# Kernel optimization log

Measured on AMD Instinct MI355X. Metric: run time of the kernel, lower is better.

Reference implementation:

```python
import jax, jax.numpy as jnp
import numpy as np

N_NODES = 100000
N_EDGES = 1600000
H_FEATS = 64


def setup_inputs() -> dict:
    key = jax.random.key(0)
    k_h, k_src, k_dst, k_w1, k_b1, k_w2, k_b2 = jax.random.split(key, 7)
    h = jax.random.normal(k_h, (N_NODES, H_FEATS), dtype=jnp.float32)
    src = jax.random.randint(k_src, (N_EDGES,), 0, N_NODES, dtype=jnp.int64)
    dst = jax.random.randint(k_dst, (N_EDGES,), 0, N_NODES, dtype=jnp.int64)
    # Linear params (torch Linear: y = x @ W.T + b). Store as [in, out] for jnp.
    lim1 = 1.0 / np.sqrt(2 * H_FEATS)
    W1 = jax.random.uniform(k_w1, (2 * H_FEATS, H_FEATS), minval=-lim1, maxval=lim1, dtype=jnp.float32)
    b1 = jax.random.uniform(k_b1, (H_FEATS,), minval=-lim1, maxval=lim1, dtype=jnp.float32)
    lim2 = 1.0 / np.sqrt(H_FEATS)
    W2 = jax.random.uniform(k_w2, (H_FEATS, 1), minval=-lim2, maxval=lim2, dtype=jnp.float32)
    b2 = jax.random.uniform(k_b2, (1,), minval=-lim2, maxval=lim2, dtype=jnp.float32)
    return {"h": h, "src": src, "dst": dst, "W1": W1, "b1": b1, "W2": W2, "b2": b2}


def reference(h, src, dst, W1, b1, W2, b2):
    # Gather src/dst node features per edge, avoid materializing the concat by
    # splitting W1 into the src-half and dst-half of the contraction.
    W1s, W1d = W1[:H_FEATS], W1[H_FEATS:]            # each [h, h]
    h_src = h[src]                                    # [E, h]
    h_dst = h[dst]                                    # [E, h]
    hidden = jax.nn.relu(h_src @ W1s + h_dst @ W1d + b1)  # [E, h]
    score = (hidden @ W2 + b2)[:, 0]                  # [E]
    return score
```

## Files before the change

kernel.cpp:

```cpp
#include <hip/hip_runtime.h>
#include <hip/hip_fp16.h>


#define HF   64
#define PADH 136
#define TPB  2

typedef __attribute__((ext_vector_type(8))) short bf16x8;
typedef __attribute__((ext_vector_type(4))) float f32x4;

__device__ __forceinline__ short f2bf(float x) {
    unsigned u = __builtin_bit_cast(unsigned, x);
    unsigned r = (u + 0x7fffu + ((u >> 16) & 1u)) >> 16;
    return (short)r;
}

__global__ __launch_bounds__(256) void node_proj_kernel(
    const float* __restrict__ h, const float* __restrict__ W1,
    const float* __restrict__ b1, __half* __restrict__ P,
    __half* __restrict__ Q, int n_nodes)
{
    __shared__ __half eb[64 * PADH];

    const int tid  = threadIdx.x;
    const int wave = tid >> 6;
    const int lane = tid & 63;
    const int q    = lane >> 4;
    const int n    = lane & 15;

    bf16x8 bfrag[8][2];
    #pragma unroll
    for (int t = 0; t < 8; ++t) {
        const float* wb = W1 + ((t >= 4) ? HF * HF : 0) + (t & 3) * 16 + n;
        #pragma unroll
        for (int kb = 0; kb < 2; ++kb) {
            #pragma unroll
            for (int j = 0; j < 8; ++j)
                bfrag[t][kb][j] = f2bf(wb[(kb * 32 + q * 8 + j) * HF]);
        }
    }
    const float bias_n = b1[0 * 16 + n];
    const float bias_n1 = b1[1 * 16 + n];
    const float bias_n2 = b1[2 * 16 + n];
    const float bias_n3 = b1[3 * 16 + n];

    for (int it = 0; it < TPB; ++it) {
        const int tile = blockIdx.x * TPB + it;
        const int n0   = tile * 64;
        if (n0 >= n_nodes) break;
        const int nrow = (n_nodes - n0 < 64) ? (n_nodes - n0) : 64;

        bf16x8 a0, a1;
        {
            int row = n0 + wave * 16 + n;
            if (row >= n_nodes) row = n_nodes - 1;
            const float* hr = h + (size_t)row * HF + q * 8;
            const float4 u0 = *(const float4*)(hr);
            const float4 u1 = *(const float4*)(hr + 4);
            const float4 v0 = *(const float4*)(hr + 32);
            const float4 v1 = *(const float4*)(hr + 36);
            a0[0] = f2bf(u0.x); a0[1] = f2bf(u0.y); a0[2] = f2bf(u0.z); a0[3] = f2bf(u0.w);
            a0[4] = f2bf(u1.x); a0[5] = f2bf(u1.y); a0[6] = f2bf(u1.z); a0[7] = f2bf(u1.w);
            a1[0] = f2bf(v0.x); a1[1] = f2bf(v0.y); a1[2] = f2bf(v0.z); a1[3] = f2bf(v0.w);
            a1[4] = f2bf(v1.x); a1[5] = f2bf(v1.y); a1[6] = f2bf(v1.z); a1[7] = f2bf(v1.w);
        }

        f32x4 acc[8];
        #pragma unroll
        for (int t = 0; t < 8; ++t) {
            acc[t] = (f32x4){0.f, 0.f, 0.f, 0.f};
            acc[t] = __builtin_amdgcn_mfma_f32_16x16x32_bf16(a0, bfrag[t][0], acc[t], 0, 0, 0);
            acc[t] = __builtin_amdgcn_mfma_f32_16x16x32_bf16(a1, bfrag[t][1], acc[t], 0, 0, 0);
        }

        if (it > 0) __syncthreads();

        #pragma unroll
        for (int t = 0; t < 8; ++t) {
            const float bb = (t == 0) ? bias_n : (t == 1) ? bias_n1
                           : (t == 2) ? bias_n2 : (t == 3) ? bias_n3 : 0.0f;
            #pragma unroll
            for (int r = 0; r < 4; ++r) {
                const int row = wave * 16 + q * 4 + r;
                eb[row * PADH + t * 16 + n] = __float2half(acc[t][r] + bb);
            }
        }
        __syncthreads();

        #pragma unroll
        for (int s = 0; s < 4; ++s) {
            const int idx  = tid + s * 256;
            const int row  = idx >> 4;
            const int part = idx & 15;
            if (row < nrow) {
                const uint4 v = *(const uint4*)&eb[row * PADH + part * 8];
                __half* dstp = (part < 8)
                    ? (P + (size_t)(n0 + row) * HF + part * 8)
                    : (Q + (size_t)(n0 + row) * HF + (part - 8) * 8);
                *(uint4*)dstp = v;
            }
        }
    }
}

__device__ __forceinline__ float dot8_relu(uint4 pv, uint4 qv, float4 wa, float4 wb) {
    const __half2* ph = (const __half2*)&pv;
    const __half2* qh = (const __half2*)&qv;
    const float2 p0 = __half22float2(ph[0]), q0 = __half22float2(qh[0]);
    const float2 p1 = __half22float2(ph[1]), q1 = __half22float2(qh[1]);
    const float2 p2 = __half22float2(ph[2]), q2 = __half22float2(qh[2]);
    const float2 p3 = __half22float2(ph[3]), q3 = __half22float2(qh[3]);
    float acc = 0.f;
    acc = fmaf(fmaxf(p0.x + q0.x, 0.f), wa.x, acc);
    acc = fmaf(fmaxf(p0.y + q0.y, 0.f), wa.y, acc);
    acc = fmaf(fmaxf(p1.x + q1.x, 0.f), wa.z, acc);
    acc = fmaf(fmaxf(p1.y + q1.y, 0.f), wa.w, acc);
    acc = fmaf(fmaxf(p2.x + q2.x, 0.f), wb.x, acc);
    acc = fmaf(fmaxf(p2.y + q2.y, 0.f), wb.y, acc);
    acc = fmaf(fmaxf(p3.x + q3.x, 0.f), wb.z, acc);
    acc = fmaf(fmaxf(p3.y + q3.y, 0.f), wb.w, acc);
    return acc;
}

__device__ __forceinline__ float red8(float v) {
    v += __shfl_xor(v, 4, 8);
    v += __shfl_xor(v, 2, 8);
    v += __shfl_xor(v, 1, 8);
    return v;
}

__global__ __launch_bounds__(256) void edge_score_kernel(
    const __half* __restrict__ P, const __half* __restrict__ Q,
    const int* __restrict__ src, const int* __restrict__ dst,
    const float* __restrict__ W2, const float* __restrict__ b2,
    float* __restrict__ out, int n_edges)
{
    const int tid   = blockIdx.x * 256 + threadIdx.x;
    const int sub   = threadIdx.x & 7;
    const int group = tid >> 3;
    const int j0    = sub * 8;
    const int e0    = group * 8;
    if (e0 >= n_edges) return;

    const float4 w2a = *(const float4*)(W2 + j0);
    const float4 w2b = *(const float4*)(W2 + j0 + 4);
    const float bias2 = b2[0];

    if (e0 + 8 <= n_edges) {
        const int4 sA = *(const int4*)(src + e0);
        const int4 sB = *(const int4*)(src + e0 + 4);
        const int4 dA = *(const int4*)(dst + e0);
        const int4 dB = *(const int4*)(dst + e0 + 4);

        const uint4 p0 = *(const uint4*)(P + (size_t)sA.x * HF + j0);
        const uint4 p1 = *(const uint4*)(P + (size_t)sA.y * HF + j0);
        const uint4 p2 = *(const uint4*)(P + (size_t)sA.z * HF + j0);
        const uint4 p3 = *(const uint4*)(P + (size_t)sA.w * HF + j0);
        const uint4 p4 = *(const uint4*)(P + (size_t)sB.x * HF + j0);
        const uint4 p5 = *(const uint4*)(P + (size_t)sB.y * HF + j0);
        const uint4 p6 = *(const uint4*)(P + (size_t)sB.z * HF + j0);
        const uint4 p7 = *(const uint4*)(P + (size_t)sB.w * HF + j0);
        const uint4 q0 = *(const uint4*)(Q + (size_t)dA.x * HF + j0);
        const uint4 q1 = *(const uint4*)(Q + (size_t)dA.y * HF + j0);
        const uint4 q2 = *(const uint4*)(Q + (size_t)dA.z * HF + j0);
        const uint4 q3 = *(const uint4*)(Q + (size_t)dA.w * HF + j0);
        const uint4 q4 = *(const uint4*)(Q + (size_t)dB.x * HF + j0);
        const uint4 q5 = *(const uint4*)(Q + (size_t)dB.y * HF + j0);
        const uint4 q6 = *(const uint4*)(Q + (size_t)dB.z * HF + j0);
        const uint4 q7 = *(const uint4*)(Q + (size_t)dB.w * HF + j0);

        float s0 = red8(dot8_relu(p0, q0, w2a, w2b));
        float s1 = red8(dot8_relu(p1, q1, w2a, w2b));
        float s2 = red8(dot8_relu(p2, q2, w2a, w2b));
        float s3 = red8(dot8_relu(p3, q3, w2a, w2b));
        float s4 = red8(dot8_relu(p4, q4, w2a, w2b));
        float s5 = red8(dot8_relu(p5, q5, w2a, w2b));
        float s6 = red8(dot8_relu(p6, q6, w2a, w2b));
        float s7 = red8(dot8_relu(p7, q7, w2a, w2b));

        if (sub == 0) {
            *(float4*)(out + e0)     = make_float4(s0 + bias2, s1 + bias2,
                                                   s2 + bias2, s3 + bias2);
            *(float4*)(out + e0 + 4) = make_float4(s4 + bias2, s5 + bias2,
                                                   s6 + bias2, s7 + bias2);
        }
    } else {
        for (int e = e0; e < n_edges; ++e) {
            const int s = src[e];
            const int d = dst[e];
            const uint4 pv = *(const uint4*)(P + (size_t)s * HF + j0);
            const uint4 qv = *(const uint4*)(Q + (size_t)d * HF + j0);
            float sc = red8(dot8_relu(pv, qv, w2a, w2b));
            if (sub == 0) out[e] = sc + bias2;
        }
    }
}

extern "C" void kernel_launch(void* const* d_in, const int* in_sizes, int n_in,
                              void* d_out, int out_size, void* d_ws, size_t ws_size,
                              hipStream_t stream) {
    const float* h   = (const float*)d_in[0];
    const int*   src = (const int*)d_in[1];
    const int*   dst = (const int*)d_in[2];
    const float* W1  = (const float*)d_in[3];
    const float* b1  = (const float*)d_in[4];
    const float* W2  = (const float*)d_in[5];
    const float* b2  = (const float*)d_in[6];
    float* out = (float*)d_out;

    const int n_nodes = in_sizes[0] / HF;
    const int n_edges = in_sizes[1];

    __half* P = (__half*)d_ws;
    __half* Q = P + (size_t)n_nodes * HF;

    const int ntiles   = (n_nodes + 63) / 64;
    const int nblocks1 = (ntiles + TPB - 1) / TPB;
    node_proj_kernel<<<nblocks1, 256, 0, stream>>>(h, W1, b1, P, Q, n_nodes);

    const int ngroups  = (n_edges + 7) / 8;
    const int nblocks2 = (ngroups + 31) / 32;
    edge_score_kernel<<<nblocks2, 256, 0, stream>>>(P, Q, src, dst, W2, b2, out, n_edges);
}
```

Before: 146.7 us.

## Quantize per-node projections to int8 with per-row scales for edge gathers

The node projection kernel now stores P and Q as 8-bit offset-quantized values with a per-node float scale, instead of fp16. The edge kernel gathers half as many bytes per edge and dequantizes inline before the ReLU and W2 dot product. The aim is to cut the random-gather memory traffic that dominates the edge kernel. The cost is extra scale loads and shuffles, more ALU work per element, and quantization error that may exceed tolerance.

Measured after the change: 147.8 us. No clear change (+0.8%).

```diff
diff --git a/kernel.cpp b/kernel.cpp
--- a/kernel.cpp
+++ b/kernel.cpp
@@ -2,9 +2,9 @@
 #include <hip/hip_fp16.h>
 
 
-#define HF   64
-#define PADH 136
-#define TPB  2
+#define HF    64
+#define PITCH 144
+#define TPB   2
 
 typedef __attribute__((ext_vector_type(8))) short bf16x8;
 typedef __attribute__((ext_vector_type(4))) float f32x4;
@@ -15,12 +15,19 @@
     return (short)r;
 }
 
+__device__ __forceinline__ unsigned char q8(float v, float inv) {
+    return (unsigned char)(int)rintf(fmaf(v, inv, 127.0f));
+}
+
 __global__ __launch_bounds__(256) void node_proj_kernel(
     const float* __restrict__ h, const float* __restrict__ W1,
-    const float* __restrict__ b1, __half* __restrict__ P,
-    __half* __restrict__ Q, int n_nodes)
+    const float* __restrict__ b1, unsigned char* __restrict__ P8,
+    unsigned char* __restrict__ Q8, float* __restrict__ Psc,
+    float* __restrict__ Qsc, int n_nodes)
 {
-    __shared__ __half eb[64 * PADH];
+    __shared__ unsigned char eb8[64 * PITCH];
+    __shared__ float pscl[64];
+    __shared__ float qscl[64];
 
     const int tid  = threadIdx.x;
     const int wave = tid >> 6;
@@ -39,7 +46,7 @@
                 bfrag[t][kb][j] = f2bf(wb[(kb * 32 + q * 8 + j) * HF]);
         }
     }
-    const float bias_n = b1[0 * 16 + n];
+    const float bias_n  = b1[0 * 16 + n];
     const float bias_n1 = b1[1 * 16 + n];
     const float bias_n2 = b1[2 * 16 + n];
     const float bias_n3 = b1[3 * 16 + n];
@@ -76,49 +83,96 @@
         if (it > 0) __syncthreads();
 
         #pragma unroll
-        for (int t = 0; t < 8; ++t) {
-            const float bb = (t == 0) ? bias_n : (t == 1) ? bias_n1
-                           : (t == 2) ? bias_n2 : (t == 3) ? bias_n3 : 0.0f;
+        for (int r = 0; r < 4; ++r) {
+            const int row = wave * 16 + q * 4 + r;
+            const float p0 = acc[0][r] + bias_n;
+            const float p1 = acc[1][r] + bias_n1;
+            const float p2 = acc[2][r] + bias_n2;
+            const float p3 = acc[3][r] + bias_n3;
+            const float q0 = acc[4][r], q1 = acc[5][r];
+            const float q2 = acc[6][r], q3 = acc[7][r];
+
+            float pa = fmaxf(fmaxf(__builtin_fabsf(p0), __builtin_fabsf(p1)),
+                             fmaxf(__builtin_fabsf(p2), __builtin_fabsf(p3)));
+            float qa = fmaxf(fmaxf(__builtin_fabsf(q0), __builtin_fabsf(q1)),
+                             fmaxf(__builtin_fabsf(q2), __builtin_fabsf(q3)));
             #pragma unroll
-            for (int r = 0; r < 4; ++r) {
-                const int row = wave * 16 + q * 4 + r;
-                eb[row * PADH + t * 16 + n] = __float2half(acc[t][r] + bb);
+            for (int m = 1; m < 16; m <<= 1) {
+                pa = fmaxf(pa, __shfl_xor(pa, m, 16));
+                qa = fmaxf(qa, __shfl_xor(qa, m, 16));
+            }
+            pa = fmaxf(pa, 1e-12f);
+            qa = fmaxf(qa, 1e-12f);
+            const float pinv = 127.0f / pa;
+            const float qinv = 127.0f / qa;
+
+            unsigned char* er = eb8 + row * PITCH;
+            er[ 0 + n]      = q8(p0, pinv);
+            er[16 + n]      = q8(p1, pinv);
+            er[32 + n]      = q8(p2, pinv);
+            er[48 + n]      = q8(p3, pinv);
+            er[64 +  0 + n] = q8(q0, qinv);
+            er[64 + 16 + n] = q8(q1, qinv);
+            er[64 + 32 + n] = q8(q2, qinv);
+            er[64 + 48 + n] = q8(q3, qinv);
+            if (n == 0) {
+                pscl[row] = pa * (1.0f / 127.0f);
+                qscl[row] = qa * (1.0f / 127.0f);
             }
         }
         __syncthreads();
 
         #pragma unroll
-        for (int s = 0; s < 4; ++s) {
+        for (int s = 0; s < 2; ++s) {
             const int idx  = tid + s * 256;
-            const int row  = idx >> 4;
-            const int part = idx & 15;
+            const int row  = idx >> 3;
+            const int part = idx & 7;
             if (row < nrow) {
-                const uint4 v = *(const uint4*)&eb[row * PADH + part * 8];
-                __half* dstp = (part < 8)
-                    ? (P + (size_t)(n0 + row) * HF + part * 8)
-                    : (Q + (size_t)(n0 + row) * HF + (part - 8) * 8);
+                const uint4 v = *(const uint4*)&eb8[row * PITCH + part * 16];
+                unsigned char* dstp = (part < 4)
+                    ? (P8 + (size_t)(n0 + row) * HF + part * 16)
+                    : (Q8 + (size_t)(n0 + row) * HF + (part - 4) * 16);
                 *(uint4*)dstp = v;
             }
         }
-    }
-}
-
-__device__ __forceinline__ float dot8_relu(uint4 pv, uint4 qv, float4 wa, float4 wb) {
-    const __half2* ph = (const __half2*)&pv;
-    const __half2* qh = (const __half2*)&qv;
-    const float2 p0 = __half22float2(ph[0]), q0 = __half22float2(qh[0]);
-    const float2 p1 = __half22float2(ph[1]), q1 = __half22float2(qh[1]);
-    const float2 p2 = __half22float2(ph[2]), q2 = __half22float2(qh[2]);
-    const float2 p3 = __half22float2(ph[3]), q3 = __half22float2(qh[3]);
+        if (tid < 128) {
+            const int rr = tid & 63;
+            if (rr < nrow) {
+                if (tid < 64) Psc[n0 + rr] = pscl[rr];
+                else          Qsc[n0 + rr] = qscl[rr];
+            }
+        }
+    }
+}
+
+__device__ __forceinline__ float dot8q(uint2 pv, uint2 qv, float4 wa, float4 wb,
+                                       float ps, float qs) {
+    const float C = -127.0f * (ps + qs);
     float acc = 0.f;
-    acc = fmaf(fmaxf(p0.x + q0.x, 0.f), wa.x, acc);
-    acc = fmaf(fmaxf(p0.y + q0.y, 0.f), wa.y, acc);
-    acc = fmaf(fmaxf(p1.x + q1.x, 0.f), wa.z, acc);
-    acc = fmaf(fmaxf(p1.y + q1.y, 0.f), wa.w, acc);
-    acc = fmaf(fmaxf(p2.x + q2.x, 0.f), wb.x, acc);
-    acc = fmaf(fmaxf(p2.y + q2.y, 0.f), wb.y, acc);
-    acc = fmaf(fmaxf(p3.x + q3.x, 0.f), wb.z, acc);
-    acc = fmaf(fmaxf(p3.y + q3.y, 0.f), wb.w, acc);
+    {
+        const unsigned u = pv.x, v = qv.x;
+        float x;
+        x = fmaf((float)(u & 255u),         ps, fmaf((float)(v & 255u),         qs, C));
+        acc = fmaf(fmaxf(x, 0.f), wa.x, acc);
+        x = fmaf((float)((u >> 8) & 255u),  ps, fmaf((float)((v >> 8) & 255u),  qs, C));
+        acc = fmaf(fmaxf(x, 0.f), wa.y, acc);
+        x = fmaf((float)((u >> 16) & 255u), ps, fmaf((float)((v >> 16) & 255u), qs, C));
+        acc = fmaf(fmaxf(x, 0.f), wa.z, acc);
+        x = fmaf((float)(u >> 24),          ps, fmaf((float)(v >> 24),          qs, C));
+        acc = fmaf(fmaxf(x, 0.f), wa.w, acc);
+    }
+    {
+        const unsigned u = pv.y, v = qv.y;
+        float x;
+        x = fmaf((float)(u & 255u),         ps, fmaf((float)(v & 255u),         qs, C));
+        acc = fmaf(fmaxf(x, 0.f), wb.x, acc);
+        x = fmaf((float)((u >> 8) & 255u),  ps, fmaf((float)((v >> 8) & 255u),  qs, C));
+        acc = fmaf(fmaxf(x, 0.f), wb.y, acc);
+        x = fmaf((float)((u >> 16) & 255u), ps, fmaf((float)((v >> 16) & 255u), qs, C));
+        acc = fmaf(fmaxf(x, 0.f), wb.z, acc);
+        x = fmaf((float)(u >> 24),          ps, fmaf((float)(v >> 24),          qs, C));
+        acc = fmaf(fmaxf(x, 0.f), wb.w, acc);
+    }
     return acc;
 }
 
@@ -130,7 +184,8 @@
 }
 
 __global__ __launch_bounds__(256) void edge_score_kernel(
-    const __half* __restrict__ P, const __half* __restrict__ Q,
+    const unsigned char* __restrict__ P8, const unsigned char* __restrict__ Q8,
+    const float* __restrict__ Psc, const float* __restrict__ Qsc,
     const int* __restrict__ src, const int* __restrict__ dst,
     const float* __restrict__ W2, const float* __restrict__ b2,
     float* __restrict__ out, int n_edges)
@@ -152,31 +207,34 @@
         const int4 dA = *(const int4*)(dst + e0);
         const int4 dB = *(const int4*)(dst + e0 + 4);
 
-        const uint4 p0 = *(const uint4*)(P + (size_t)sA.x * HF + j0);
-        const uint4 p1 = *(const uint4*)(P + (size_t)sA.y * HF + j0);
-        const uint4 p2 = *(const uint4*)(P + (size_t)sA.z * HF + j0);
-        const uint4 p3 = *(const uint4*)(P + (size_t)sA.w * HF + j0);
-        const uint4 p4 = *(const uint4*)(P + (size_t)sB.x * HF + j0);
-        const uint4 p5 = *(const uint4*)(P + (size_t)sB.y * HF + j0);
-        const uint4 p6 = *(const uint4*)(P + (size_t)sB.z * HF + j0);
-        const uint4 p7 = *(const uint4*)(P + (size_t)sB.w * HF + j0);
-        const uint4 q0 = *(const uint4*)(Q + (size_t)dA.x * HF + j0);
-        const uint4 q1 = *(const uint4*)(Q + (size_t)dA.y * HF + j0);
-        const uint4 q2 = *(const uint4*)(Q + (size_t)dA.z * HF + j0);
-        const uint4 q3 = *(const uint4*)(Q + (size_t)dA.w * HF + j0);
-        const uint4 q4 = *(const uint4*)(Q + (size_t)dB.x * HF + j0);
-        const uint4 q5 = *(const uint4*)(Q + (size_t)dB.y * HF + j0);
-        const uint4 q6 = *(const uint4*)(Q + (size_t)dB.z * HF + j0);
-        const uint4 q7 = *(const uint4*)(Q + (size_t)dB.w * HF + j0);
-
-        float s0 = red8(dot8_relu(p0, q0, w2a, w2b));
-        float s1 = red8(dot8_relu(p1, q1, w2a, w2b));
-        float s2 = red8(dot8_relu(p2, q2, w2a, w2b));
-        float s3 = red8(dot8_relu(p3, q3, w2a, w2b));
-        float s4 = red8(dot8_relu(p4, q4, w2a, w2b));
-        float s5 = red8(dot8_relu(p5, q5, w2a, w2b));
-        float s6 = red8(dot8_relu(p6, q6, w2a, w2b));
-        float s7 = red8(dot8_relu(p7, q7, w2a, w2b));
+        const float ps_own = Psc[src[e0 + sub]];
+        const float qs_own = Qsc[dst[e0 + sub]];
+
+        const uint2 p0 = *(const uint2*)(P8 + (size_t)sA.x * HF + j0);
+        const uint2 p1 = *(const uint2*)(P8 + (size_t)sA.y * HF + j0);
+        const uint2 p2 = *(const uint2*)(P8 + (size_t)sA.z * HF + j0);
+        const uint2 p3 = *(const uint2*)(P8 + (size_t)sA.w * HF + j0);
+        const uint2 p4 = *(const uint2*)(P8 + (size_t)sB.x * HF + j0);
+        const uint2 p5 = *(const uint2*)(P8 + (size_t)sB.y * HF + j0);
+        const uint2 p6 = *(const uint2*)(P8 + (size_t)sB.z * HF + j0);
+        const uint2 p7 = *(const uint2*)(P8 + (size_t)sB.w * HF + j0);
+        const uint2 q0 = *(const uint2*)(Q8 + (size_t)dA.x * HF + j0);
+        const uint2 q1 = *(const uint2*)(Q8 + (size_t)dA.y * HF + j0);
+        const uint2 q2 = *(const uint2*)(Q8 + (size_t)dA.z * HF + j0);
+        const uint2 q3 = *(const uint2*)(Q8 + (size_t)dA.w * HF + j0);
+        const uint2 q4 = *(const uint2*)(Q8 + (size_t)dB.x * HF + j0);
+        const uint2 q5 = *(const uint2*)(Q8 + (size_t)dB.y * HF + j0);
+        const uint2 q6 = *(const uint2*)(Q8 + (size_t)dB.z * HF + j0);
+        const uint2 q7 = *(const uint2*)(Q8 + (size_t)dB.w * HF + j0);
+
+        float s0 = red8(dot8q(p0, q0, w2a, w2b, __shfl(ps_own, 0, 8), __shfl(qs_own, 0, 8)));
+        float s1 = red8(dot8q(p1, q1, w2a, w2b, __shfl(ps_own, 1, 8), __shfl(qs_own, 1, 8)));
+        float s2 = red8(dot8q(p2, q2, w2a, w2b, __shfl(ps_own, 2, 8), __shfl(qs_own, 2, 8)));
+        float s3 = red8(dot8q(p3, q3, w2a, w2b, __shfl(ps_own, 3, 8), __shfl(qs_own, 3, 8)));
+        float s4 = red8(dot8q(p4, q4, w2a, w2b, __shfl(ps_own, 4, 8), __shfl(qs_own, 4, 8)));
+        float s5 = red8(dot8q(p5, q5, w2a, w2b, __shfl(ps_own, 5, 8), __shfl(qs_own, 5, 8)));
+        float s6 = red8(dot8q(p6, q6, w2a, w2b, __shfl(ps_own, 6, 8), __shfl(qs_own, 6, 8)));
+        float s7 = red8(dot8q(p7, q7, w2a, w2b, __shfl(ps_own, 7, 8), __shfl(qs_own, 7, 8)));
 
         if (sub == 0) {
             *(float4*)(out + e0)     = make_float4(s0 + bias2, s1 + bias2,
@@ -188,9 +246,11 @@
         for (int e = e0; e < n_edges; ++e) {
             const int s = src[e];
             const int d = dst[e];
-            const uint4 pv = *(const uint4*)(P + (size_t)s * HF + j0);
-            const uint4 qv = *(const uint4*)(Q + (size_t)d * HF + j0);
-            float sc = red8(dot8_relu(pv, qv, w2a, w2b));
+            const float ps = Psc[s];
+            const float qs = Qsc[d];
+            const uint2 pv = *(const uint2*)(P8 + (size_t)s * HF + j0);
+            const uint2 qv = *(const uint2*)(Q8 + (size_t)d * HF + j0);
+            float sc = red8(dot8q(pv, qv, w2a, w2b, ps, qs));
             if (sub == 0) out[e] = sc + bias2;
         }
     }
@@ -211,14 +271,16 @@
     const int n_nodes = in_sizes[0] / HF;
     const int n_edges = in_sizes[1];
 
-    __half* P = (__half*)d_ws;
-    __half* Q = P + (size_t)n_nodes * HF;
+    unsigned char* P8 = (unsigned char*)d_ws;
+    unsigned char* Q8 = P8 + (size_t)n_nodes * HF;
+    float* Psc = (float*)(Q8 + (size_t)n_nodes * HF);
+    float* Qsc = Psc + n_nodes;
 
     const int ntiles   = (n_nodes + 63) / 64;
     const int nblocks1 = (ntiles + TPB - 1) / TPB;
-    node_proj_kernel<<<nblocks1, 256, 0, stream>>>(h, W1, b1, P, Q, n_nodes);
+    node_proj_kernel<<<nblocks1, 256, 0, stream>>>(h, W1, b1, P8, Q8, Psc, Qsc, n_nodes);
 
     const int ngroups  = (n_edges + 7) / 8;
     const int nblocks2 = (ngroups + 31) / 32;
-    edge_score_kernel<<<nblocks2, 256, 0, stream>>>(P, Q, src, dst, W2, b2, out, n_edges);
-}
+    edge_score_kernel<<<nblocks2, 256, 0, stream>>>(P8, Q8, Psc, Qsc, src, dst, W2, b2, out, n_edges);
+}
```
